# Optimization experiments

Measured on AMD Instinct MI355X. Metric: run time of the kernel, lower is better.

## Reference

```python
import jax, jax.numpy as jnp
import numpy as np

B, N, D, OUT = 4, 512, 128, 128

def setup_inputs() -> dict:
    key = jax.random.key(0)
    k1, k2, k3, k4 = jax.random.split(key, 4)
    x = jax.random.normal(k1, (B, N, D), dtype=jnp.float32)
    # binary adjacency mask (float, as it multiplies edge features in the original)
    adj = (jax.random.uniform(k2, (B, N, N)) < 0.5).astype(jnp.float32)
    # nn.Linear(2D, OUT): store as (2D, OUT) so y = feat @ W + b
    W = jax.random.normal(k3, (2 * D, OUT), dtype=jnp.float32) * (1.0 / np.sqrt(2 * D))
    b = jax.random.normal(k4, (OUT,), dtype=jnp.float32) * 0.01
    return {"x": x, "adj": adj, "W": W, "b": b}

def reference(x, adj, W, b):
    # edge_feat = cat([x_i, x_j - x_i]); linear on concat decomposes as
    # x_i @ W1 + (x_j - x_i) @ W2 = x_i @ (W1 - W2) + x_j @ W2  -> avoids the (B,N,N,2D) concat.
    d = x.shape[-1]
    W1, W2 = W[:d], W[d:]
    p = jnp.einsum('bnd,do->bno', x, W1 - W2)   # contribution of x_i
    q = jnp.einsum('bnd,do->bno', x, W2)        # contribution of x_j
    pre = p[:, :, None, :] + q[:, None, :, :] + b  # (B, N, N, OUT)
    h = jax.nn.relu(pre) * adj[..., None]          # dropout is identity in eval mode
    return jnp.max(h, axis=2)                      # max over neighbors j -> (B, N, OUT)
```

## Files before the change

kernel.cpp:

```cpp
#include <hip/hip_runtime.h>

#define B_ 4
#define N_ 512
#define D_ 128
#define O_ 128

#define R1 8

__global__ __launch_bounds__(1024)
void gemm_pq_kernel(const float* __restrict__ x, const float* __restrict__ W,
                    const float* __restrict__ bias, float* __restrict__ q,
                    float* __restrict__ phat) {
    const int tid = threadIdx.x;
    const int o   = tid & (O_ - 1);
    const int kq  = __builtin_amdgcn_readfirstlane(tid >> 7);
    const int row0 = blockIdx.x * R1;

    const float* __restrict__ xb = x + (size_t)row0 * D_;

    float accp[R1], accq[R1];
#pragma unroll
    for (int r = 0; r < R1; ++r) { accp[r] = 0.0f; accq[r] = 0.0f; }

    const int k0 = kq * (D_ / 8);
#pragma unroll 4
    for (int k = k0; k < k0 + D_ / 8; ++k) {
        const float w1 = W[(size_t)k * O_ + o];
        const float w2 = W[(size_t)(k + D_) * O_ + o];
        const float wd = w1 - w2;
#pragma unroll
        for (int r = 0; r < R1; ++r) {
            const float xv = xb[(size_t)r * D_ + k];
            accp[r] = fmaf(xv, wd, accp[r]);
            accq[r] = fmaf(xv, w2, accq[r]);
        }
    }

    __shared__ float redq[R1][O_][9];
    __shared__ float redp[R1][O_][9];

#pragma unroll
    for (int r = 0; r < R1; ++r) {
        redq[r][o][kq] = accq[r];
        redp[r][o][kq] = accp[r];
    }
    __syncthreads();

    {
        const int rr = tid >> 7;
        const int oo = tid & (O_ - 1);
        const float sq = ((redq[rr][oo][0] + redq[rr][oo][1]) +
                          (redq[rr][oo][2] + redq[rr][oo][3])) +
                         ((redq[rr][oo][4] + redq[rr][oo][5]) +
                          (redq[rr][oo][6] + redq[rr][oo][7]));
        const float sp = ((redp[rr][oo][0] + redp[rr][oo][1]) +
                          (redp[rr][oo][2] + redp[rr][oo][3])) +
                         ((redp[rr][oo][4] + redp[rr][oo][5]) +
                          (redp[rr][oo][6] + redp[rr][oo][7]));
        const size_t idx = (size_t)(row0 + rr) * O_ + oo;
        q[idx]    = sq;
        phat[idx] = sp + bias[oo];
    }
}

#define TI 8
#define JS 8
#define JB 16

__global__ __launch_bounds__(1024)
void maskmax_kernel(const float* __restrict__ q, const float* __restrict__ phat,
                    const float* __restrict__ adj, float* __restrict__ out) {
    const int tid = threadIdx.x;
    const int o   = tid & (O_ - 1);
    const int jq  = __builtin_amdgcn_readfirstlane(tid >> 7);
    const int b   = blockIdx.x >> 6;
    const int i0  = (blockIdx.x & 63) * TI;

    const float* __restrict__ qb   = q + (size_t)b * N_ * O_ + o;
    const float* __restrict__ arow = adj + ((size_t)b * N_ + i0) * N_;

    float m[TI];
#pragma unroll
    for (int i = 0; i < TI; ++i) m[i] = -1e30f;

    const int j0   = jq * (N_ / JS);
    const int jend = j0 + (N_ / JS);

    float qv[JB], qn[JB];
#pragma unroll
    for (int u = 0; u < JB; ++u)
        qv[u] = qb[(size_t)(j0 + u) * O_];

    for (int j = j0; j < jend; j += JB) {
        const int jn = (j + JB < jend) ? (j + JB) : j0;
#pragma unroll
        for (int u = 0; u < JB; ++u)
            qn[u] = qb[(size_t)(jn + u) * O_];

#pragma unroll
        for (int i = 0; i < TI; ++i) {
            const float* __restrict__ ar = arow + (size_t)i * N_ + j;
            float c[JB];
#pragma unroll
            for (int u = 0; u < JB; ++u)
                c[u] = fmaf(ar[u], 1024.0f, qv[u]);
            float mi = m[i];
#pragma unroll
            for (int u = 0; u < JB; u += 4) {
                mi = fmaxf(mi, fmaxf(c[u],     c[u + 1]));
                mi = fmaxf(mi, fmaxf(c[u + 2], c[u + 3]));
            }
            m[i] = mi;
        }

#pragma unroll
        for (int u = 0; u < JB; ++u) qv[u] = qn[u];
    }

    __shared__ float part[TI][O_][JS + 1];
#pragma unroll
    for (int i = 0; i < TI; ++i) part[i][o][jq] = m[i];
    __syncthreads();

    {
        const int i  = tid >> 7;
        const int oo = tid & (O_ - 1);
        float mm = -1e30f;
#pragma unroll
        for (int p = 0; p < JS; ++p) mm = fmaxf(mm, part[i][oo][p]);
        const size_t idx = ((size_t)b * N_ + i0 + i) * O_ + oo;
        const float v = phat[idx] + mm - 1024.0f;
        out[idx] = v > 0.0f ? v : 0.0f;
    }
}

extern "C" void kernel_launch(void* const* d_in, const int* in_sizes, int n_in,
                              void* d_out, int out_size, void* d_ws, size_t ws_size,
                              hipStream_t stream) {
    const float* x    = (const float*)d_in[0];
    const float* adj  = (const float*)d_in[1];
    const float* W    = (const float*)d_in[2];
    const float* bias = (const float*)d_in[3];
    float* out = (float*)d_out;

    float* q    = (float*)d_ws;
    float* phat = q + (size_t)B_ * N_ * O_;

    gemm_pq_kernel<<<(B_ * N_) / R1, 1024, 0, stream>>>(x, W, bias, q, phat);
    maskmax_kernel<<<B_ * (N_ / TI), 1024, 0, stream>>>(q, phat, adj, out);
}
```

Before: 73.02 us.

## Fuse GEMM and masked-max kernels into one cooperative kernel with grid sync

Merges the projection GEMM and the masked neighbor-max into a single cooperative kernel separated by a grid-wide barrier. Each block's GEMM rows coincide with its output rows, so phat stays in a register instead of going through a global buffer. The aim is to drop one kernel launch and the phat round trip. In exchange it adds a grid-sync cost, needs all 256 blocks of 1024 threads co-resident, and reuses the shared buffers across phases.

Result: slower. 170.2 us (+133.1%).

```diff
diff --git a/kernel.cpp b/kernel.cpp
--- a/kernel.cpp
+++ b/kernel.cpp
@@ -1,4 +1,7 @@
 #include <hip/hip_runtime.h>
+#include <hip/hip_cooperative_groups.h>
+
+namespace cg = cooperative_groups;
 
 #define B_ 4
 #define N_ 512
@@ -6,131 +9,132 @@
 #define O_ 128
 
 #define R1 8
-
-__global__ __launch_bounds__(1024)
-void gemm_pq_kernel(const float* __restrict__ x, const float* __restrict__ W,
-                    const float* __restrict__ bias, float* __restrict__ q,
-                    float* __restrict__ phat) {
-    const int tid = threadIdx.x;
-    const int o   = tid & (O_ - 1);
-    const int kq  = __builtin_amdgcn_readfirstlane(tid >> 7);
-    const int row0 = blockIdx.x * R1;
-
-    const float* __restrict__ xb = x + (size_t)row0 * D_;
-
-    float accp[R1], accq[R1];
-#pragma unroll
-    for (int r = 0; r < R1; ++r) { accp[r] = 0.0f; accq[r] = 0.0f; }
-
-    const int k0 = kq * (D_ / 8);
-#pragma unroll 4
-    for (int k = k0; k < k0 + D_ / 8; ++k) {
-        const float w1 = W[(size_t)k * O_ + o];
-        const float w2 = W[(size_t)(k + D_) * O_ + o];
-        const float wd = w1 - w2;
-#pragma unroll
-        for (int r = 0; r < R1; ++r) {
-            const float xv = xb[(size_t)r * D_ + k];
-            accp[r] = fmaf(xv, wd, accp[r]);
-            accq[r] = fmaf(xv, w2, accq[r]);
-        }
-    }
-
-    __shared__ float redq[R1][O_][9];
-    __shared__ float redp[R1][O_][9];
-
-#pragma unroll
-    for (int r = 0; r < R1; ++r) {
-        redq[r][o][kq] = accq[r];
-        redp[r][o][kq] = accp[r];
-    }
-    __syncthreads();
-
-    {
-        const int rr = tid >> 7;
-        const int oo = tid & (O_ - 1);
-        const float sq = ((redq[rr][oo][0] + redq[rr][oo][1]) +
-                          (redq[rr][oo][2] + redq[rr][oo][3])) +
-                         ((redq[rr][oo][4] + redq[rr][oo][5]) +
-                          (redq[rr][oo][6] + redq[rr][oo][7]));
-        const float sp = ((redp[rr][oo][0] + redp[rr][oo][1]) +
-                          (redp[rr][oo][2] + redp[rr][oo][3])) +
-                         ((redp[rr][oo][4] + redp[rr][oo][5]) +
-                          (redp[rr][oo][6] + redp[rr][oo][7]));
-        const size_t idx = (size_t)(row0 + rr) * O_ + oo;
-        q[idx]    = sq;
-        phat[idx] = sp + bias[oo];
-    }
-}
-
 #define TI 8
 #define JS 8
 #define JB 16
 
-__global__ __launch_bounds__(1024)
-void maskmax_kernel(const float* __restrict__ q, const float* __restrict__ phat,
-                    const float* __restrict__ adj, float* __restrict__ out) {
+__global__ __launch_bounds__(1024, 4)
+void fused_edgeconv(const float* __restrict__ x, const float* __restrict__ adj,
+                    const float* __restrict__ W, const float* __restrict__ bias,
+                    float* __restrict__ q, float* __restrict__ out) {
     const int tid = threadIdx.x;
-    const int o   = tid & (O_ - 1);
-    const int jq  = __builtin_amdgcn_readfirstlane(tid >> 7);
-    const int b   = blockIdx.x >> 6;
-    const int i0  = (blockIdx.x & 63) * TI;
+    const int bid = blockIdx.x;
 
-    const float* __restrict__ qb   = q + (size_t)b * N_ * O_ + o;
-    const float* __restrict__ arow = adj + ((size_t)b * N_ + i0) * N_;
+    __shared__ float bufA[R1][O_][9];
+    __shared__ float bufB[R1][O_][9];
 
-    float m[TI];
+    float phat_reg;
+    {
+        const int o  = tid & (O_ - 1);
+        const int kq = __builtin_amdgcn_readfirstlane(tid >> 7);
+        const int row0 = bid * R1;
+        const float* __restrict__ xb = x + (size_t)row0 * D_;
+
+        float accp[R1], accq[R1];
 #pragma unroll
-    for (int i = 0; i < TI; ++i) m[i] = -1e30f;
+        for (int r = 0; r < R1; ++r) { accp[r] = 0.0f; accq[r] = 0.0f; }
 
-    const int j0   = jq * (N_ / JS);
-    const int jend = j0 + (N_ / JS);
-
-    float qv[JB], qn[JB];
+        const int k0 = kq * (D_ / 8);
+#pragma unroll 4
+        for (int k = k0; k < k0 + D_ / 8; ++k) {
+            const float w1 = W[(size_t)k * O_ + o];
+            const float w2 = W[(size_t)(k + D_) * O_ + o];
+            const float wd = w1 - w2;
 #pragma unroll
-    for (int u = 0; u < JB; ++u)
-        qv[u] = qb[(size_t)(j0 + u) * O_];
-
-    for (int j = j0; j < jend; j += JB) {
-        const int jn = (j + JB < jend) ? (j + JB) : j0;
-#pragma unroll
-        for (int u = 0; u < JB; ++u)
-            qn[u] = qb[(size_t)(jn + u) * O_];
-
-#pragma unroll
-        for (int i = 0; i < TI; ++i) {
-            const float* __restrict__ ar = arow + (size_t)i * N_ + j;
-            float c[JB];
-#pragma unroll
-            for (int u = 0; u < JB; ++u)
-                c[u] = fmaf(ar[u], 1024.0f, qv[u]);
-            float mi = m[i];
-#pragma unroll
-            for (int u = 0; u < JB; u += 4) {
-                mi = fmaxf(mi, fmaxf(c[u],     c[u + 1]));
-                mi = fmaxf(mi, fmaxf(c[u + 2], c[u + 3]));
+            for (int r = 0; r < R1; ++r) {
+                const float xv = xb[(size_t)r * D_ + k];
+                accp[r] = fmaf(xv, wd, accp[r]);
+                accq[r] = fmaf(xv, w2, accq[r]);
             }
-            m[i] = mi;
         }
 
 #pragma unroll
-        for (int u = 0; u < JB; ++u) qv[u] = qn[u];
+        for (int r = 0; r < R1; ++r) {
+            bufA[r][o][kq] = accq[r];
+            bufB[r][o][kq] = accp[r];
+        }
+        __syncthreads();
+
+        {
+            const int rr = tid >> 7;
+            const int oo = tid & (O_ - 1);
+            const float sq = ((bufA[rr][oo][0] + bufA[rr][oo][1]) +
+                              (bufA[rr][oo][2] + bufA[rr][oo][3])) +
+                             ((bufA[rr][oo][4] + bufA[rr][oo][5]) +
+                              (bufA[rr][oo][6] + bufA[rr][oo][7]));
+            const float sp = ((bufB[rr][oo][0] + bufB[rr][oo][1]) +
+                              (bufB[rr][oo][2] + bufB[rr][oo][3])) +
+                             ((bufB[rr][oo][4] + bufB[rr][oo][5]) +
+                              (bufB[rr][oo][6] + bufB[rr][oo][7]));
+            q[(size_t)(row0 + rr) * O_ + oo] = sq;
+            phat_reg = sp + bias[oo];
+        }
     }
 
-    __shared__ float part[TI][O_][JS + 1];
-#pragma unroll
-    for (int i = 0; i < TI; ++i) part[i][o][jq] = m[i];
-    __syncthreads();
+    __threadfence();
+    cg::this_grid().sync();
 
     {
-        const int i  = tid >> 7;
-        const int oo = tid & (O_ - 1);
-        float mm = -1e30f;
+        const int o  = tid & (O_ - 1);
+        const int jq = __builtin_amdgcn_readfirstlane(tid >> 7);
+        const int b  = bid >> 6;
+        const int i0 = (bid & 63) * TI;
+
+        const float* __restrict__ qb   = q + (size_t)b * N_ * O_ + o;
+        const float* __restrict__ arow = adj + ((size_t)b * N_ + i0) * N_;
+
+        float m[TI];
 #pragma unroll
-        for (int p = 0; p < JS; ++p) mm = fmaxf(mm, part[i][oo][p]);
-        const size_t idx = ((size_t)b * N_ + i0 + i) * O_ + oo;
-        const float v = phat[idx] + mm - 1024.0f;
-        out[idx] = v > 0.0f ? v : 0.0f;
+        for (int i = 0; i < TI; ++i) m[i] = -1e30f;
+
+        const int j0   = jq * (N_ / JS);
+        const int jend = j0 + (N_ / JS);
+
+        float qv[JB], qn[JB];
+#pragma unroll
+        for (int u = 0; u < JB; ++u)
+            qv[u] = qb[(size_t)(j0 + u) * O_];
+
+        for (int j = j0; j < jend; j += JB) {
+            const int jn = (j + JB < jend) ? (j + JB) : j0;
+#pragma unroll
+            for (int u = 0; u < JB; ++u)
+                qn[u] = qb[(size_t)(jn + u) * O_];
+
+#pragma unroll
+            for (int i = 0; i < TI; ++i) {
+                const float* __restrict__ ar = arow + (size_t)i * N_ + j;
+                float c[JB];
+#pragma unroll
+                for (int u = 0; u < JB; ++u)
+                    c[u] = fmaf(ar[u], 1024.0f, qv[u]);
+                float mi = m[i];
+#pragma unroll
+                for (int u = 0; u < JB; u += 4) {
+                    mi = fmaxf(mi, fmaxf(c[u],     c[u + 1]));
+                    mi = fmaxf(mi, fmaxf(c[u + 2], c[u + 3]));
+                }
+                m[i] = mi;
+            }
+
+#pragma unroll
+            for (int u = 0; u < JB; ++u) qv[u] = qn[u];
+        }
+
+        __syncthreads();
+#pragma unroll
+        for (int i = 0; i < TI; ++i) bufA[i][o][jq] = m[i];
+        __syncthreads();
+
+        {
+            const int i  = tid >> 7;
+            const int oo = tid & (O_ - 1);
+            float mm = -1e30f;
+#pragma unroll
+            for (int p = 0; p < JS; ++p) mm = fmaxf(mm, bufA[i][oo][p]);
+            const float v = phat_reg + mm - 1024.0f;
+            out[((size_t)b * N_ + i0 + i) * O_ + oo] = v > 0.0f ? v : 0.0f;
+        }
     }
 }
 
@@ -143,9 +147,11 @@
     const float* bias = (const float*)d_in[3];
     float* out = (float*)d_out;
 
-    float* q    = (float*)d_ws;
-    float* phat = q + (size_t)B_ * N_ * O_;
+    float* q = (float*)d_ws;
 
-    gemm_pq_kernel<<<(B_ * N_) / R1, 1024, 0, stream>>>(x, W, bias, q, phat);
-    maskmax_kernel<<<B_ * (N_ / TI), 1024, 0, stream>>>(q, phat, adj, out);
+    void* args[] = { (void*)&x, (void*)&adj, (void*)&W, (void*)&bias,
+                     (void*)&q, (void*)&out };
+    hipLaunchCooperativeKernel((void*)fused_edgeconv,
+                               dim3((B_ * N_) / R1), dim3(1024),
+                               args, 0, stream);
 }
```

## Give each thread two output columns and split the reduction into sixteen slices

Applied to the files above, without the earlier changes.

Both kernels now map each thread to a pair of adjacent output columns loaded as float2, and use sixteen wavefront-sized slices over k (GEMM) or j (mask-max) instead of eight. The mask-max kernel loads all 32 q rows of its slice into registers up front, dropping the double-buffered loop, so each adjacency value feeds two outputs. The shared-memory partial buffers are transposed to [slice][column] with padding for float2 writes. This halves scalar adj loads per output and widens memory accesses, at the cost of more register pressure and a longer final cross-slice reduction.

New measurement: 77.60 us. 6.3% more time.

```diff
diff --git a/kernel.cpp b/kernel.cpp
--- a/kernel.cpp
+++ b/kernel.cpp
@@ -12,51 +12,61 @@
                     const float* __restrict__ bias, float* __restrict__ q,
                     float* __restrict__ phat) {
     const int tid = threadIdx.x;
-    const int o   = tid & (O_ - 1);
-    const int kq  = __builtin_amdgcn_readfirstlane(tid >> 7);
+    const int o2  = (tid & 63) * 2;
+    const int kq  = __builtin_amdgcn_readfirstlane(tid >> 6);
     const int row0 = blockIdx.x * R1;
+    const int k0   = kq * 8;
 
     const float* __restrict__ xb = x + (size_t)row0 * D_;
 
-    float accp[R1], accq[R1];
+    float2 w1v[8], w2v[8];
 #pragma unroll
-    for (int r = 0; r < R1; ++r) { accp[r] = 0.0f; accq[r] = 0.0f; }
+    for (int kk = 0; kk < 8; ++kk) {
+        w1v[kk] = *(const float2*)&W[(size_t)(k0 + kk) * O_ + o2];
+        w2v[kk] = *(const float2*)&W[(size_t)(k0 + kk + D_) * O_ + o2];
+    }
+    float2 wd[8];
+#pragma unroll
+    for (int kk = 0; kk < 8; ++kk) {
+        wd[kk].x = w1v[kk].x - w2v[kk].x;
+        wd[kk].y = w1v[kk].y - w2v[kk].y;
+    }
 
-    const int k0 = kq * (D_ / 8);
-#pragma unroll 4
-    for (int k = k0; k < k0 + D_ / 8; ++k) {
-        const float w1 = W[(size_t)k * O_ + o];
-        const float w2 = W[(size_t)(k + D_) * O_ + o];
-        const float wd = w1 - w2;
+    float accp[R1][2], accq[R1][2];
 #pragma unroll
-        for (int r = 0; r < R1; ++r) {
-            const float xv = xb[(size_t)r * D_ + k];
-            accp[r] = fmaf(xv, wd, accp[r]);
-            accq[r] = fmaf(xv, w2, accq[r]);
+    for (int r = 0; r < R1; ++r) {
+        accp[r][0] = 0.0f; accp[r][1] = 0.0f;
+        accq[r][0] = 0.0f; accq[r][1] = 0.0f;
+    }
+
+#pragma unroll
+    for (int r = 0; r < R1; ++r) {
+#pragma unroll
+        for (int kk = 0; kk < 8; ++kk) {
+            const float xv = xb[(size_t)r * D_ + k0 + kk];
+            accp[r][0] = fmaf(xv, wd[kk].x,  accp[r][0]);
+            accp[r][1] = fmaf(xv, wd[kk].y,  accp[r][1]);
+            accq[r][0] = fmaf(xv, w2v[kk].x, accq[r][0]);
+            accq[r][1] = fmaf(xv, w2v[kk].y, accq[r][1]);
         }
     }
 
-    __shared__ float redq[R1][O_][9];
-    __shared__ float redp[R1][O_][9];
+    __shared__ float redq[R1][16][O_ + 2];
+    __shared__ float redp[R1][16][O_ + 2];
 
 #pragma unroll
     for (int r = 0; r < R1; ++r) {
-        redq[r][o][kq] = accq[r];
-        redp[r][o][kq] = accp[r];
+        *(float2*)&redq[r][kq][o2] = make_float2(accq[r][0], accq[r][1]);
+        *(float2*)&redp[r][kq][o2] = make_float2(accp[r][0], accp[r][1]);
     }
     __syncthreads();
 
     {
         const int rr = tid >> 7;
         const int oo = tid & (O_ - 1);
-        const float sq = ((redq[rr][oo][0] + redq[rr][oo][1]) +
-                          (redq[rr][oo][2] + redq[rr][oo][3])) +
-                         ((redq[rr][oo][4] + redq[rr][oo][5]) +
-                          (redq[rr][oo][6] + redq[rr][oo][7]));
-        const float sp = ((redp[rr][oo][0] + redp[rr][oo][1]) +
-                          (redp[rr][oo][2] + redp[rr][oo][3])) +
-                         ((redp[rr][oo][4] + redp[rr][oo][5]) +
-                          (redp[rr][oo][6] + redp[rr][oo][7]));
+        float sq = 0.0f, sp = 0.0f;
+#pragma unroll
+        for (int p = 0; p < 16; ++p) { sq += redq[rr][p][oo]; sp += redp[rr][p][oo]; }
         const size_t idx = (size_t)(row0 + rr) * O_ + oo;
         q[idx]    = sq;
         phat[idx] = sp + bias[oo];
@@ -64,62 +74,50 @@
 }
 
 #define TI 8
-#define JS 8
-#define JB 16
 
 __global__ __launch_bounds__(1024)
 void maskmax_kernel(const float* __restrict__ q, const float* __restrict__ phat,
                     const float* __restrict__ adj, float* __restrict__ out) {
     const int tid = threadIdx.x;
-    const int o   = tid & (O_ - 1);
-    const int jq  = __builtin_amdgcn_readfirstlane(tid >> 7);
+    const int o2  = (tid & 63) * 2;
+    const int jq  = __builtin_amdgcn_readfirstlane(tid >> 6);
     const int b   = blockIdx.x >> 6;
     const int i0  = (blockIdx.x & 63) * TI;
+    const int j0  = jq * 32;
 
-    const float* __restrict__ qb   = q + (size_t)b * N_ * O_ + o;
-    const float* __restrict__ arow = adj + ((size_t)b * N_ + i0) * N_;
+    const float* __restrict__ qb   = q + (size_t)b * N_ * O_ + o2;
+    const float* __restrict__ arow = adj + ((size_t)b * N_ + i0) * N_ + j0;
 
-    float m[TI];
+    float2 qv[32];
 #pragma unroll
-    for (int i = 0; i < TI; ++i) m[i] = -1e30f;
+    for (int u = 0; u < 32; ++u)
+        qv[u] = *(const float2*)&qb[(size_t)(j0 + u) * O_];
 
-    const int j0   = jq * (N_ / JS);
-    const int jend = j0 + (N_ / JS);
-
-    float qv[JB], qn[JB];
+    float m[TI][2];
 #pragma unroll
-    for (int u = 0; u < JB; ++u)
-        qv[u] = qb[(size_t)(j0 + u) * O_];
-
-    for (int j = j0; j < jend; j += JB) {
-        const int jn = (j + JB < jend) ? (j + JB) : j0;
-#pragma unroll
-        for (int u = 0; u < JB; ++u)
-            qn[u] = qb[(size_t)(jn + u) * O_];
+    for (int i = 0; i < TI; ++i) { m[i][0] = -1e30f; m[i][1] = -1e30f; }
 
 #pragma unroll
-        for (int i = 0; i < TI; ++i) {
-            const float* __restrict__ ar = arow + (size_t)i * N_ + j;
-            float c[JB];
+    for (int i = 0; i < TI; ++i) {
+        const float* __restrict__ ar = arow + (size_t)i * N_;
+        float mx = m[i][0], my = m[i][1];
 #pragma unroll
-            for (int u = 0; u < JB; ++u)
-                c[u] = fmaf(ar[u], 1024.0f, qv[u]);
-            float mi = m[i];
-#pragma unroll
-            for (int u = 0; u < JB; u += 4) {
-                mi = fmaxf(mi, fmaxf(c[u],     c[u + 1]));
-                mi = fmaxf(mi, fmaxf(c[u + 2], c[u + 3]));
-            }
-            m[i] = mi;
+        for (int u = 0; u < 32; u += 2) {
+            const float a0 = ar[u], a1 = ar[u + 1];
+            const float c0x = fmaf(a0, 1024.0f, qv[u].x);
+            const float c0y = fmaf(a0, 1024.0f, qv[u].y);
+            const float c1x = fmaf(a1, 1024.0f, qv[u + 1].x);
+            const float c1y = fmaf(a1, 1024.0f, qv[u + 1].y);
+            mx = fmaxf(mx, fmaxf(c0x, c1x));
+            my = fmaxf(my, fmaxf(c0y, c1y));
         }
-
-#pragma unroll
-        for (int u = 0; u < JB; ++u) qv[u] = qn[u];
+        m[i][0] = mx; m[i][1] = my;
     }
 
-    __shared__ float part[TI][O_][JS + 1];
+    __shared__ float part[TI][16][O_ + 2];
 #pragma unroll
-    for (int i = 0; i < TI; ++i) part[i][o][jq] = m[i];
+    for (int i = 0; i < TI; ++i)
+        *(float2*)&part[i][jq][o2] = make_float2(m[i][0], m[i][1]);
     __syncthreads();
 
     {
@@ -127,7 +125,7 @@
         const int oo = tid & (O_ - 1);
         float mm = -1e30f;
 #pragma unroll
-        for (int p = 0; p < JS; ++p) mm = fmaxf(mm, part[i][oo][p]);
+        for (int p = 0; p < 16; ++p) mm = fmaxf(mm, part[i][p][oo]);
         const size_t idx = ((size_t)b * N_ + i0 + i) * O_ + oo;
         const float v = phat[idx] + mm - 1024.0f;
         out[idx] = v > 0.0f ? v : 0.0f;
```
